# Kernel tuning notes

Hardware: AMD Instinct MI355X
Metric: run time of the kernel (lower is better)

The kernel has to match this reference:

```python
import jax, jax.numpy as jnp
import numpy as np

N_NODES = 50000
N_EDGES = 800000
IN_CH = 64
HEADS = 8
OUT_CH = 8
LEAKY_ALPHA = 0.3  # Keras LeakyReLU default


def setup_inputs() -> dict:
    key = jax.random.key(0)
    k1, k2, k3, k4, k5 = jax.random.split(key, 5)
    h = jax.random.normal(k1, (N_NODES, IN_CH), dtype=jnp.float32)
    W = jax.random.normal(k2, (2 * IN_CH, HEADS * OUT_CH), dtype=jnp.float32) * 0.1
    a = jax.random.normal(k3, (1, HEADS * OUT_CH), dtype=jnp.float32) * 0.1
    src = jax.random.randint(k4, (N_EDGES,), 0, N_NODES, dtype=jnp.int32)
    tgt = jax.random.randint(k5, (N_EDGES,), 0, N_NODES, dtype=jnp.int32)
    return {"h": h, "W": W, "a": a, "src": src, "tgt": tgt}


def reference(h, W, a, src, tgt):
    # h: [N, C]; W: [2C, H*D]; a: [1, H*D]; src/tgt: [E]
    N = h.shape[0]
    hi = h[src]                                   # [E, C] gather source feats
    hj = h[tgt]                                   # [E, C] gather target feats
    hij = jnp.concatenate([hi, hj], axis=-1)      # [E, 2C]
    e = jax.nn.leaky_relu(hij @ W, negative_slope=LEAKY_ALPHA)  # [E, H*D]
    # (dropout omitted: eval mode)
    e = e * a                                     # broadcast attention vector
    e = e.reshape(-1, HEADS, OUT_CH).sum(axis=-1)  # [E, H] per-head logits
    # segment softmax over target nodes (numerically stable)
    m = jax.ops.segment_max(e, tgt, num_segments=N)   # [N, H]
    ex = jnp.exp(e - m[tgt])                          # [E, H]
    s = jax.ops.segment_sum(ex, tgt, num_segments=N)  # [N, H]
    att = ex / s[tgt]                                 # [E, H]
    # weight source features per head (in_channel == head*out_channel branch)
    msg = hi.reshape(-1, HEADS, OUT_CH) * att[:, :, None]  # [E, H, D]
    out = jax.ops.segment_sum(msg.reshape(-1, HEADS * OUT_CH), tgt, num_segments=N)
    return out  # [N, H*D]
```

## Files before the change

kernel.cpp:

```cpp
#include <hip/hip_runtime.h>
#include <hip/hip_fp16.h>
#include <math.h>

#define ALPHA 0.3f
#define MAXDEG 64
#define LOG2E 1.44269504088896f
#define UVOFF (64 * 68 + 4)
#define NSLICE 128

__device__ __forceinline__ unsigned int pack2(float u, float hv) {
    __half2 p = __floats2half2_rn(u, hv);
    unsigned int w;
    __builtin_memcpy(&w, &p, 4);
    return w;
}

__device__ __forceinline__ float2 unpack2(unsigned int w) {
    __half2 p;
    __builtin_memcpy(&p, &w, 4);
    return __half22float2(p);
}

__device__ __forceinline__ float dpp_sum8(float z) {
    int t;
    t = __builtin_amdgcn_mov_dpp(__float_as_int(z), 0xB1, 0xF, 0xF, true);
    z += __int_as_float(t);
    t = __builtin_amdgcn_mov_dpp(__float_as_int(z), 0x4E, 0xF, 0xF, true);
    z += __int_as_float(t);
    t = __builtin_amdgcn_mov_dpp(__float_as_int(z), 0x141, 0xF, 0xF, true);
    z += __int_as_float(t);
    return z;
}

__global__ __launch_bounds__(256) void k_uv(const float* __restrict__ h,
                                            const float* __restrict__ W,
                                            unsigned int* __restrict__ g,
                                            float* __restrict__ vbuf,
                                            int* __restrict__ cursor, int N) {
    __shared__ float Ws[UVOFF + 64 * 68];
    const int t = threadIdx.x;
    const int gidx = blockIdx.x * 256 + t;
    if (gidx < N) cursor[gidx] = 0;

    for (int i = t; i < 128 * 64; i += 256) {
        const int row = i >> 6, col = i & 63;
        const int idx = (row < 64) ? (row * 68 + col) : (UVOFF + (row - 64) * 68 + col);
        Ws[idx] = W[i];
    }
    __syncthreads();

    const int nb = blockIdx.x * 64;
    const int kk = t & 15;
    const int gn = t >> 4;
    const int colbase = (kk * 8) & 63;
    const int wbase   = (kk < 8) ? 0 : UVOFF;

    int nidx[4];
#pragma unroll
    for (int i = 0; i < 4; ++i) {
        int n = nb + gn * 4 + i;
        nidx[i] = (n < N) ? n : (N - 1);
    }

    float acc[4][8];
#pragma unroll
    for (int i = 0; i < 4; ++i)
#pragma unroll
        for (int j = 0; j < 8; ++j) acc[i][j] = 0.0f;

    for (int c4 = 0; c4 < 64; c4 += 4) {
        float hh[4][4];
#pragma unroll
        for (int i = 0; i < 4; ++i) {
            const float4 tv = *(const float4*)&h[(size_t)nidx[i] * 64 + c4];
            hh[i][0] = tv.x; hh[i][1] = tv.y; hh[i][2] = tv.z; hh[i][3] = tv.w;
        }
#pragma unroll
        for (int cc = 0; cc < 4; ++cc) {
            const float* wrow = &Ws[wbase + (c4 + cc) * 68 + colbase];
            const float4 w0 = *(const float4*)(wrow);
            const float4 w1 = *(const float4*)(wrow + 4);
            const float wv[8] = {w0.x, w0.y, w0.z, w0.w, w1.x, w1.y, w1.z, w1.w};
#pragma unroll
            for (int i = 0; i < 4; ++i)
#pragma unroll
                for (int j = 0; j < 8; ++j) acc[i][j] += hh[i][cc] * wv[j];
        }
    }

#pragma unroll
    for (int i = 0; i < 4; ++i) {
        const int n = nb + gn * 4 + i;
        if (n >= N) continue;
        if (kk < 8) {
            const float4 h0 = *(const float4*)&h[(size_t)n * 64 + colbase];
            const float4 h1 = *(const float4*)&h[(size_t)n * 64 + colbase + 4];
            const float hv[8] = {h0.x, h0.y, h0.z, h0.w, h1.x, h1.y, h1.z, h1.w};
            unsigned int w[8];
#pragma unroll
            for (int j = 0; j < 8; ++j) w[j] = pack2(acc[i][j], hv[j]);
            uint4 w0 = {w[0], w[1], w[2], w[3]};
            uint4 w1 = {w[4], w[5], w[6], w[7]};
            *(uint4*)&g[(size_t)n * 64 + colbase]     = w0;
            *(uint4*)&g[(size_t)n * 64 + colbase + 4] = w1;
        } else {
            float4 o0 = {acc[i][0], acc[i][1], acc[i][2], acc[i][3]};
            float4 o1 = {acc[i][4], acc[i][5], acc[i][6], acc[i][7]};
            *(float4*)&vbuf[(size_t)n * 64 + colbase]     = o0;
            *(float4*)&vbuf[(size_t)n * 64 + colbase + 4] = o1;
        }
    }
}

__global__ __launch_bounds__(256) void k_fill(const int* __restrict__ src,
                                              const int* __restrict__ tgt,
                                              int* __restrict__ cursor,
                                              unsigned short* __restrict__ srcs, int E) {
    const int p  = blockIdx.x & 7;
    const int sl = blockIdx.x >> 3;
    const int Q  = E >> 2;
    const int per = (Q + NSLICE - 1) / NSLICE;
    const int q0 = sl * per;
    const int q1 = min(q0 + per, Q);

    for (int q = q0 + (int)threadIdx.x; q < q1; q += 256) {
        const int4 s4 = ((const int4*)src)[q];
        const int4 t4 = ((const int4*)tgt)[q];
        if ((t4.x & 7) == p) { const int pos = atomicAdd(&cursor[t4.x], 1); if (pos < MAXDEG) srcs[(size_t)t4.x * MAXDEG + pos] = (unsigned short)s4.x; }
        if ((t4.y & 7) == p) { const int pos = atomicAdd(&cursor[t4.y], 1); if (pos < MAXDEG) srcs[(size_t)t4.y * MAXDEG + pos] = (unsigned short)s4.y; }
        if ((t4.z & 7) == p) { const int pos = atomicAdd(&cursor[t4.z], 1); if (pos < MAXDEG) srcs[(size_t)t4.z * MAXDEG + pos] = (unsigned short)s4.z; }
        if ((t4.w & 7) == p) { const int pos = atomicAdd(&cursor[t4.w], 1); if (pos < MAXDEG) srcs[(size_t)t4.w * MAXDEG + pos] = (unsigned short)s4.w; }
    }
    if (sl == 0) {
        for (int i = (Q << 2) + (int)threadIdx.x; i < E; i += 256) {
            const int ti = tgt[i];
            if ((ti & 7) == p) {
                const int pos = atomicAdd(&cursor[ti], 1);
                if (pos < MAXDEG) srcs[(size_t)ti * MAXDEG + pos] = (unsigned short)src[i];
            }
        }
    }
}

__global__ __launch_bounds__(256) void k_node(const unsigned int* __restrict__ g,
                                              const float* __restrict__ vbuf,
                                              const float* __restrict__ a,
                                              const int* __restrict__ cnt,
                                              const unsigned short* __restrict__ srcs,
                                              float* __restrict__ out, int N) {
    const int wid  = (blockIdx.x * 256 + threadIdx.x) >> 6;
    const int lane = threadIdx.x & 63;
    if (wid >= N) return;

    const float v_l = vbuf[(size_t)wid * 64 + lane];
    const float a_l = a[lane] * LOG2E;
    const int num = min(cnt[wid], MAXDEG);
    const int beg = wid * MAXDEG;

    float l_run = 0.0f, acc = 0.0f;

    int k = 0;
    for (; k + 8 <= num; k += 8) {
        const ushort4 sa = *(const ushort4*)(srcs + beg + k);
        const ushort4 sb = *(const ushort4*)(srcs + beg + k + 4);
        unsigned int w[8];
        w[0] = g[(size_t)sa.x * 64 + lane];
        w[1] = g[(size_t)sa.y * 64 + lane];
        w[2] = g[(size_t)sa.z * 64 + lane];
        w[3] = g[(size_t)sa.w * 64 + lane];
        w[4] = g[(size_t)sb.x * 64 + lane];
        w[5] = g[(size_t)sb.y * 64 + lane];
        w[6] = g[(size_t)sb.z * 64 + lane];
        w[7] = g[(size_t)sb.w * 64 + lane];
#pragma unroll
        for (int j = 0; j < 8; ++j) {
            const float2 f = unpack2(w[j]);
            const float q = f.x + v_l;
            float z = fmaxf(q, q * ALPHA) * a_l;
            z = dpp_sum8(z);
            const float p = __builtin_amdgcn_exp2f(z);
            l_run += p;
            acc = fmaf(f.y, p, acc);
        }
    }
    if (k + 4 <= num) {
        const ushort4 sa = *(const ushort4*)(srcs + beg + k);
        unsigned int w[4];
        w[0] = g[(size_t)sa.x * 64 + lane];
        w[1] = g[(size_t)sa.y * 64 + lane];
        w[2] = g[(size_t)sa.z * 64 + lane];
        w[3] = g[(size_t)sa.w * 64 + lane];
#pragma unroll
        for (int j = 0; j < 4; ++j) {
            const float2 f = unpack2(w[j]);
            const float q = f.x + v_l;
            float z = fmaxf(q, q * ALPHA) * a_l;
            z = dpp_sum8(z);
            const float p = __builtin_amdgcn_exp2f(z);
            l_run += p;
            acc = fmaf(f.y, p, acc);
        }
        k += 4;
    }
    for (; k < num; ++k) {
        const int s = srcs[beg + k];
        const float2 f = unpack2(g[(size_t)s * 64 + lane]);
        const float q = f.x + v_l;
        float z = fmaxf(q, q * ALPHA) * a_l;
        z = dpp_sum8(z);
        const float p = __builtin_amdgcn_exp2f(z);
        l_run += p;
        acc = fmaf(f.y, p, acc);
    }

    out[(size_t)wid * 64 + lane] = (num > 0) ? (acc / l_run) : 0.0f;
}

extern "C" void kernel_launch(void* const* d_in, const int* in_sizes, int n_in,
                              void* d_out, int out_size, void* d_ws, size_t ws_size,
                              hipStream_t stream) {
    const float* h   = (const float*)d_in[0];
    const float* W   = (const float*)d_in[1];
    const float* a   = (const float*)d_in[2];
    const int*   src = (const int*)d_in[3];
    const int*   tgt = (const int*)d_in[4];
    float* out = (float*)d_out;

    const int N = in_sizes[0] / 64;
    const int E = in_sizes[3];

    unsigned int*   g      = (unsigned int*)d_ws;
    float*          vbuf   = (float*)(g + (size_t)N * 64);
    int*            cursor = (int*)(vbuf + (size_t)N * 64);
    unsigned short* srcs   = (unsigned short*)(cursor + N);

    k_uv<<<(N + 63) / 64, 256, 0, stream>>>(h, W, g, vbuf, cursor, N);
    k_fill<<<8 * NSLICE, 256, 0, stream>>>(src, tgt, cursor, srcs, E);
    k_node<<<((size_t)N * 64 + 255) / 256, 256, 0, stream>>>(g, vbuf, a, cursor, srcs, out, N);
}
```

Baseline: 99.37 us.

## Partition cursor/adjacency buckets by target residue and use persistent node waves

Reindexes the per-target cursor and adjacency arrays so that each residue class (tgt & 7) occupies a contiguous range. The fill blocks for one class then touch a compact region, which should give better cache locality for their atomics and stores. The fill loop now loads tgt first and skips the src load when no lane in the int4 matches. The node kernel becomes a grid-stride persistent kernel with 2048 blocks and remaps each node id to its bucket index, which adds index arithmetic and may reduce latency hiding compared with one wave per node.

```diff
diff --git a/kernel.cpp b/kernel.cpp
--- a/kernel.cpp
+++ b/kernel.cpp
@@ -36,11 +36,12 @@
                                             const float* __restrict__ W,
                                             unsigned int* __restrict__ g,
                                             float* __restrict__ vbuf,
-                                            int* __restrict__ cursor, int N) {
+                                            int* __restrict__ cursor,
+                                            int N, int NC) {
     __shared__ float Ws[UVOFF + 64 * 68];
     const int t = threadIdx.x;
     const int gidx = blockIdx.x * 256 + t;
-    if (gidx < N) cursor[gidx] = 0;
+    if (gidx < NC) cursor[gidx] = 0;
 
     for (int i = t; i < 128 * 64; i += 256) {
         const int row = i >> 6, col = i & 63;
@@ -115,28 +116,36 @@
 __global__ __launch_bounds__(256) void k_fill(const int* __restrict__ src,
                                               const int* __restrict__ tgt,
                                               int* __restrict__ cursor,
-                                              unsigned short* __restrict__ srcs, int E) {
+                                              unsigned short* __restrict__ srcs,
+                                              int E, int NPB) {
     const int p  = blockIdx.x & 7;
     const int sl = blockIdx.x >> 3;
     const int Q  = E >> 2;
     const int per = (Q + NSLICE - 1) / NSLICE;
     const int q0 = sl * per;
     const int q1 = min(q0 + per, Q);
+    const int pbase = p * NPB;
 
     for (int q = q0 + (int)threadIdx.x; q < q1; q += 256) {
+        const int4 t4 = ((const int4*)tgt)[q];
+        const bool m0 = (t4.x & 7) == p;
+        const bool m1 = (t4.y & 7) == p;
+        const bool m2 = (t4.z & 7) == p;
+        const bool m3 = (t4.w & 7) == p;
+        if (!(m0 | m1 | m2 | m3)) continue;
         const int4 s4 = ((const int4*)src)[q];
-        const int4 t4 = ((const int4*)tgt)[q];
-        if ((t4.x & 7) == p) { const int pos = atomicAdd(&cursor[t4.x], 1); if (pos < MAXDEG) srcs[(size_t)t4.x * MAXDEG + pos] = (unsigned short)s4.x; }
-        if ((t4.y & 7) == p) { const int pos = atomicAdd(&cursor[t4.y], 1); if (pos < MAXDEG) srcs[(size_t)t4.y * MAXDEG + pos] = (unsigned short)s4.y; }
-        if ((t4.z & 7) == p) { const int pos = atomicAdd(&cursor[t4.z], 1); if (pos < MAXDEG) srcs[(size_t)t4.z * MAXDEG + pos] = (unsigned short)s4.z; }
-        if ((t4.w & 7) == p) { const int pos = atomicAdd(&cursor[t4.w], 1); if (pos < MAXDEG) srcs[(size_t)t4.w * MAXDEG + pos] = (unsigned short)s4.w; }
+        if (m0) { const int b = pbase + (t4.x >> 3); const int pos = atomicAdd(&cursor[b], 1); if (pos < MAXDEG) srcs[(size_t)b * MAXDEG + pos] = (unsigned short)s4.x; }
+        if (m1) { const int b = pbase + (t4.y >> 3); const int pos = atomicAdd(&cursor[b], 1); if (pos < MAXDEG) srcs[(size_t)b * MAXDEG + pos] = (unsigned short)s4.y; }
+        if (m2) { const int b = pbase + (t4.z >> 3); const int pos = atomicAdd(&cursor[b], 1); if (pos < MAXDEG) srcs[(size_t)b * MAXDEG + pos] = (unsigned short)s4.z; }
+        if (m3) { const int b = pbase + (t4.w >> 3); const int pos = atomicAdd(&cursor[b], 1); if (pos < MAXDEG) srcs[(size_t)b * MAXDEG + pos] = (unsigned short)s4.w; }
     }
     if (sl == 0) {
         for (int i = (Q << 2) + (int)threadIdx.x; i < E; i += 256) {
             const int ti = tgt[i];
             if ((ti & 7) == p) {
-                const int pos = atomicAdd(&cursor[ti], 1);
-                if (pos < MAXDEG) srcs[(size_t)ti * MAXDEG + pos] = (unsigned short)src[i];
+                const int b = pbase + (ti >> 3);
+                const int pos = atomicAdd(&cursor[b], 1);
+                if (pos < MAXDEG) srcs[(size_t)b * MAXDEG + pos] = (unsigned short)src[i];
             }
         }
     }
@@ -147,34 +156,67 @@
                                               const float* __restrict__ a,
                                               const int* __restrict__ cnt,
                                               const unsigned short* __restrict__ srcs,
-                                              float* __restrict__ out, int N) {
-    const int wid  = (blockIdx.x * 256 + threadIdx.x) >> 6;
+                                              float* __restrict__ out,
+                                              int N, int NPB) {
     const int lane = threadIdx.x & 63;
-    if (wid >= N) return;
-
-    const float v_l = vbuf[(size_t)wid * 64 + lane];
+    const int wv0  = (blockIdx.x * 256 + threadIdx.x) >> 6;
+    const int nwv  = gridDim.x * 4;
     const float a_l = a[lane] * LOG2E;
-    const int num = min(cnt[wid], MAXDEG);
-    const int beg = wid * MAXDEG;
-
-    float l_run = 0.0f, acc = 0.0f;
-
-    int k = 0;
-    for (; k + 8 <= num; k += 8) {
-        const ushort4 sa = *(const ushort4*)(srcs + beg + k);
-        const ushort4 sb = *(const ushort4*)(srcs + beg + k + 4);
-        unsigned int w[8];
-        w[0] = g[(size_t)sa.x * 64 + lane];
-        w[1] = g[(size_t)sa.y * 64 + lane];
-        w[2] = g[(size_t)sa.z * 64 + lane];
-        w[3] = g[(size_t)sa.w * 64 + lane];
-        w[4] = g[(size_t)sb.x * 64 + lane];
-        w[5] = g[(size_t)sb.y * 64 + lane];
-        w[6] = g[(size_t)sb.z * 64 + lane];
-        w[7] = g[(size_t)sb.w * 64 + lane];
-#pragma unroll
-        for (int j = 0; j < 8; ++j) {
-            const float2 f = unpack2(w[j]);
+
+    for (int wid = wv0; wid < N; wid += nwv) {
+        const int b   = (wid & 7) * NPB + (wid >> 3);
+        const float v_l = vbuf[(size_t)wid * 64 + lane];
+        const int num = min(cnt[b], MAXDEG);
+        const int beg = b * MAXDEG;
+
+        float l_run = 0.0f, acc = 0.0f;
+
+        int k = 0;
+        for (; k + 8 <= num; k += 8) {
+            const ushort4 sa = *(const ushort4*)(srcs + beg + k);
+            const ushort4 sb = *(const ushort4*)(srcs + beg + k + 4);
+            unsigned int w[8];
+            w[0] = g[(size_t)sa.x * 64 + lane];
+            w[1] = g[(size_t)sa.y * 64 + lane];
+            w[2] = g[(size_t)sa.z * 64 + lane];
+            w[3] = g[(size_t)sa.w * 64 + lane];
+            w[4] = g[(size_t)sb.x * 64 + lane];
+            w[5] = g[(size_t)sb.y * 64 + lane];
+            w[6] = g[(size_t)sb.z * 64 + lane];
+            w[7] = g[(size_t)sb.w * 64 + lane];
+#pragma unroll
+            for (int j = 0; j < 8; ++j) {
+                const float2 f = unpack2(w[j]);
+                const float q = f.x + v_l;
+                float z = fmaxf(q, q * ALPHA) * a_l;
+                z = dpp_sum8(z);
+                const float p = __builtin_amdgcn_exp2f(z);
+                l_run += p;
+                acc = fmaf(f.y, p, acc);
+            }
+        }
+        if (k + 4 <= num) {
+            const ushort4 sa = *(const ushort4*)(srcs + beg + k);
+            unsigned int w[4];
+            w[0] = g[(size_t)sa.x * 64 + lane];
+            w[1] = g[(size_t)sa.y * 64 + lane];
+            w[2] = g[(size_t)sa.z * 64 + lane];
+            w[3] = g[(size_t)sa.w * 64 + lane];
+#pragma unroll
+            for (int j = 0; j < 4; ++j) {
+                const float2 f = unpack2(w[j]);
+                const float q = f.x + v_l;
+                float z = fmaxf(q, q * ALPHA) * a_l;
+                z = dpp_sum8(z);
+                const float p = __builtin_amdgcn_exp2f(z);
+                l_run += p;
+                acc = fmaf(f.y, p, acc);
+            }
+            k += 4;
+        }
+        for (; k < num; ++k) {
+            const int s = srcs[beg + k];
+            const float2 f = unpack2(g[(size_t)s * 64 + lane]);
             const float q = f.x + v_l;
             float z = fmaxf(q, q * ALPHA) * a_l;
             z = dpp_sum8(z);
@@ -182,38 +224,9 @@
             l_run += p;
             acc = fmaf(f.y, p, acc);
         }
-    }
-    if (k + 4 <= num) {
-        const ushort4 sa = *(const ushort4*)(srcs + beg + k);
-        unsigned int w[4];
-        w[0] = g[(size_t)sa.x * 64 + lane];
-        w[1] = g[(size_t)sa.y * 64 + lane];
-        w[2] = g[(size_t)sa.z * 64 + lane];
-        w[3] = g[(size_t)sa.w * 64 + lane];
-#pragma unroll
-        for (int j = 0; j < 4; ++j) {
-            const float2 f = unpack2(w[j]);
-            const float q = f.x + v_l;
-            float z = fmaxf(q, q * ALPHA) * a_l;
-            z = dpp_sum8(z);
-            const float p = __builtin_amdgcn_exp2f(z);
-            l_run += p;
-            acc = fmaf(f.y, p, acc);
-        }
-        k += 4;
-    }
-    for (; k < num; ++k) {
-        const int s = srcs[beg + k];
-        const float2 f = unpack2(g[(size_t)s * 64 + lane]);
-        const float q = f.x + v_l;
-        float z = fmaxf(q, q * ALPHA) * a_l;
-        z = dpp_sum8(z);
-        const float p = __builtin_amdgcn_exp2f(z);
-        l_run += p;
-        acc = fmaf(f.y, p, acc);
-    }
-
-    out[(size_t)wid * 64 + lane] = (num > 0) ? (acc / l_run) : 0.0f;
+
+        out[(size_t)wid * 64 + lane] = (num > 0) ? (acc / l_run) : 0.0f;
+    }
 }
 
 extern "C" void kernel_launch(void* const* d_in, const int* in_sizes, int n_in,
@@ -228,13 +241,15 @@
 
     const int N = in_sizes[0] / 64;
     const int E = in_sizes[3];
+    const int NPB = (N + 7) / 8;
+    const int NC  = NPB * 8;
 
     unsigned int*   g      = (unsigned int*)d_ws;
     float*          vbuf   = (float*)(g + (size_t)N * 64);
     int*            cursor = (int*)(vbuf + (size_t)N * 64);
-    unsigned short* srcs   = (unsigned short*)(cursor + N);
-
-    k_uv<<<(N + 63) / 64, 256, 0, stream>>>(h, W, g, vbuf, cursor, N);
-    k_fill<<<8 * NSLICE, 256, 0, stream>>>(src, tgt, cursor, srcs, E);
-    k_node<<<((size_t)N * 64 + 255) / 256, 256, 0, stream>>>(g, vbuf, a, cursor, srcs, out, N);
-}
+    unsigned short* srcs   = (unsigned short*)(cursor + NC);
+
+    k_uv<<<(N + 63) / 64, 256, 0, stream>>>(h, W, g, vbuf, cursor, N, NC);
+    k_fill<<<8 * NSLICE, 256, 0, stream>>>(src, tgt, cursor, srcs, E, NPB);
+    k_node<<<2048, 256, 0, stream>>>(g, vbuf, a, cursor, srcs, out, N, NPB);
+}
```

New measurement: 100.7 us. No clear change (+1.3%).
